# Kernel optimization log

Hardware: AMD Instinct MI355X
Metric: run time of the kernel (lower is better)

The kernel has to match this reference:

```python
import jax, jax.numpy as jnp
import numpy as np

NUM_HEADS = 16


def _local_attn(q, k, v, bias, nq, nk):
    """Blocked local attention, faithful to rearrange_to_dense_trunk semantics.
    q,k,v: [B,H,N,D]; bias: [B,Hb,N,N] (Hb broadcasts against H).
    Trunk i (queries [i*nq,(i+1)*nq)) attends keys at original indices
    [i*nq - pad_left, i*nq - pad_left + nk); out-of-range keys/values/bias are
    zero-padded (the module pads with zeros, no -inf key masking).
    Assumes N % nq == 0 (q_pad_length == 0, so the query mask loop is a no-op).
    """
    B, H, N, D = q.shape
    T = N // nq                      # n_trunks
    pad_left = (nk - nq) // 2
    Lp = (T - 1) * nq + nk           # padded key length so every window is full
    pad_right = Lp - pad_left - N
    k_p = jnp.pad(k, ((0, 0), (0, 0), (pad_left, pad_right), (0, 0)))
    v_p = jnp.pad(v, ((0, 0), (0, 0), (pad_left, pad_right), (0, 0)))
    b_p = jnp.pad(bias, ((0, 0), (0, 0), (0, 0), (pad_left, pad_right)))
    # window gather indices: [T, nk]
    kidx = jnp.arange(T)[:, None] * nq + jnp.arange(nk)[None, :]
    k_t = k_p[:, :, kidx, :]         # [B,H,T,nk,D]
    v_t = v_p[:, :, kidx, :]         # [B,H,T,nk,D]
    Bb, Hb = bias.shape[0], bias.shape[1]
    b_r = b_p.reshape(Bb, Hb, T, nq, Lp)
    b_t = jnp.take_along_axis(b_r, kidx[None, None, :, None, :], axis=-1)  # [Bb,Hb,T,nq,nk]
    q_t = q.reshape(B, H, T, nq, D)
    scores = jnp.einsum('bhtqd,bhtkd->bhtqk', q_t, k_t) + b_t
    w = jax.nn.softmax(scores, axis=-1)
    o = jnp.einsum('bhtqk,bhtkd->bhtqd', w, v_t)
    return o.reshape(B, H, N, D)


def setup_inputs() -> dict:
    key = jax.random.key(0)
    ks = jax.random.split(key, 8)
    B, N, C = 1, 4096, 256
    H, D = NUM_HEADS, 64
    HD = H * D
    q_x = jax.random.normal(ks[0], (B, N, C), dtype=jnp.float32)
    kv_x = jax.random.normal(ks[1], (B, N, C), dtype=jnp.float32)
    attn_bias = jax.random.normal(ks[2], (B, 1, N, N), dtype=jnp.float32) * 0.1
    Wq = jax.random.normal(ks[3], (C, HD), dtype=jnp.float32) / np.sqrt(C).astype(np.float32)
    Wk = jax.random.normal(ks[4], (C, HD), dtype=jnp.float32) / np.sqrt(C).astype(np.float32)
    Wv = jax.random.normal(ks[5], (C, HD), dtype=jnp.float32) / np.sqrt(C).astype(np.float32)
    Wg = jax.random.normal(ks[6], (C, HD), dtype=jnp.float32) / np.sqrt(C).astype(np.float32)
    Wo = jax.random.normal(ks[7], (HD, C), dtype=jnp.float32) / np.sqrt(HD).astype(np.float32)
    return {"q_x": q_x, "kv_x": kv_x, "attn_bias": attn_bias,
            "Wq": Wq, "Wk": Wk, "Wv": Wv, "Wg": Wg, "Wo": Wo,
            "n_queries": 64, "n_keys": 256}


def reference(q_x, kv_x, attn_bias, Wq, Wk, Wv, Wg, Wo, n_queries, n_keys):
    B, N, C = q_x.shape
    H = NUM_HEADS
    D = Wq.shape[-1] // H
    def split_heads(x):
        return x.reshape(B, N, H, D).transpose(0, 2, 1, 3)  # [B,H,N,D]
    q = split_heads(q_x @ Wq) / jnp.sqrt(jnp.float32(D))
    k = split_heads(kv_x @ Wk)
    v = split_heads(kv_x @ Wv)
    o = _local_attn(q, k, v, attn_bias, n_queries, n_keys)
    o = o.transpose(0, 2, 1, 3).reshape(B, N, H * D)
    g = jax.nn.sigmoid(q_x @ Wg)  # gating head
    return (o * g) @ Wo
```

## Files before the change

### kernel.cpp

```cpp
#include <hip/hip_runtime.h>

#define N_ 4096
#define C_ 256
#define H_ 16
#define D_ 64
#define HD_ 1024

typedef __attribute__((ext_vector_type(8))) _Float16 f16x8;
typedef __attribute__((ext_vector_type(4))) _Float16 f16x4;
typedef __attribute__((ext_vector_type(4))) float f32x4;

__device__ __forceinline__ void gload16(const void* g, void* l) {
    __builtin_amdgcn_global_load_lds(
        (const __attribute__((address_space(1))) unsigned int*)g,
        (__attribute__((address_space(3))) unsigned int*)l, 16, 0, 0);
}

__global__ __launch_bounds__(256) void convert_kernel(
    const float* __restrict__ q_x, const float* __restrict__ kv_x,
    const float* __restrict__ Wq, const float* __restrict__ Wk,
    const float* __restrict__ Wv, const float* __restrict__ Wg,
    const float* __restrict__ Wo,
    _Float16* __restrict__ Xf, _Float16* __restrict__ WTf,
    _Float16* __restrict__ WoTf)
{
    __shared__ float ts[64][65];
    const int b = blockIdx.x;
    const int tid = threadIdx.x;

    if (b < 512) {
        const int seg = b >> 8;
        const float* src = seg ? kv_x : q_x;
        _Float16* df = Xf + (size_t)seg * 1048576;
        const int base = (b & 255) * 4096 + tid * 16;
#pragma unroll
        for (int q = 0; q < 4; ++q) {
            float4 v = *(const float4*)&src[base + q * 4];
            f16x4 fv;
            fv[0] = (_Float16)v.x; fv[1] = (_Float16)v.y;
            fv[2] = (_Float16)v.z; fv[3] = (_Float16)v.w;
            *(f16x4*)&df[base + q * 4] = fv;
        }
        return;
    }

    const float* src;
    _Float16* df;
    int srcC, dstC, r0, c0;
    if (b < 768) {
        const int widx = (b - 512) >> 6;
        const int tile = (b - 512) & 63;
        src = (widx == 0) ? Wq : (widx == 1) ? Wk : (widx == 2) ? Wv : Wg;
        df = WTf + (size_t)widx * 262144;
        srcC = 1024; dstC = 256;
        r0 = (tile >> 4) * 64;
        c0 = (tile & 15) * 64;
    } else {
        const int tile = b - 768;
        src = Wo; df = WoTf;
        srcC = 256; dstC = 1024;
        r0 = (tile >> 2) * 64;
        c0 = (tile & 3) * 64;
    }
    {
        const int r = tid >> 2;
        const int cch = (tid & 3) * 16;
#pragma unroll
        for (int q = 0; q < 4; ++q) {
            float4 v = *(const float4*)&src[(size_t)(r0 + r) * srcC + c0 + cch + q * 4];
            ts[r][cch + q * 4 + 0] = v.x;
            ts[r][cch + q * 4 + 1] = v.y;
            ts[r][cch + q * 4 + 2] = v.z;
            ts[r][cch + q * 4 + 3] = v.w;
        }
    }
    __syncthreads();
    {
        const int c = tid >> 2;
        const int rch = (tid & 3) * 16;
#pragma unroll
        for (int q = 0; q < 4; ++q) {
            f16x4 fv;
#pragma unroll
            for (int j = 0; j < 4; ++j)
                fv[j] = (_Float16)ts[rch + q * 4 + j][c];
            *(f16x4*)&df[(size_t)(c0 + c) * dstC + r0 + rch + q * 4] = fv;
        }
    }
}

__global__ __launch_bounds__(256) void proj_mfma(
    const _Float16* __restrict__ Xf, const _Float16* __restrict__ WTf,
    _Float16* __restrict__ qh, _Float16* __restrict__ kh,
    _Float16* __restrict__ vh, _Float16* __restrict__ gh)
{
    __shared__ __align__(16) char psmem[34816];
    _Float16* As = (_Float16*)psmem;
    _Float16* Bs = (_Float16*)(psmem + 16384);

    const int lb  = blockIdx.x;
    const int xcd = lb & 7;
    const int gr  = (lb >> 6) * 8 + xcd;
    const int g   = gr >> 5;
    const int m0  = (gr & 31) * 128;
    const int c0  = ((lb >> 3) & 7) * 128;

    const _Float16* A = Xf + ((g == 1 || g == 2) ? 1048576 : 0);
    const _Float16* B = WTf + (size_t)g * 262144;

    const int tid  = threadIdx.x;
    const int wave = tid >> 6;
    const int lane = tid & 63;
    const int wr   = wave >> 1;
    const int wc   = wave & 1;
    const int frow = lane & 15;
    const int grp  = lane >> 4;

    f32x4 acc[4][4];
#pragma unroll
    for (int i = 0; i < 4; ++i)
#pragma unroll
        for (int j = 0; j < 4; ++j) acc[i][j] = (f32x4){0.f, 0.f, 0.f, 0.f};

    const int srow = tid >> 3;
    const int sch  = tid & 7;

    for (int kt = 0; kt < 256; kt += 64) {
        __syncthreads();
#pragma unroll
        for (int p = 0; p < 4; ++p) {
            const int row = p * 32 + srow;
            const int koff = kt + ((sch ^ (row & 7)) << 3);
            gload16(A + (size_t)(m0 + row) * 256 + koff, (char*)As + p * 4096 + tid * 16);
            gload16(B + (size_t)(c0 + row) * 256 + koff, (char*)Bs + p * 4096 + tid * 16);
        }
        __syncthreads();

#pragma unroll
        for (int ks = 0; ks < 2; ++ks) {
            f16x8 af[4], bf[4];
#pragma unroll
            for (int f = 0; f < 4; ++f) {
                const int ra = wr * 64 + f * 16 + frow;
                const int rb = wc * 64 + f * 16 + frow;
                af[f] = *(const f16x8*)((char*)As + ra * 128 + (((ks * 4 + grp) ^ (ra & 7)) << 4));
                bf[f] = *(const f16x8*)((char*)Bs + rb * 128 + (((ks * 4 + grp) ^ (rb & 7)) << 4));
            }
#pragma unroll
            for (int i = 0; i < 4; ++i)
#pragma unroll
                for (int j = 0; j < 4; ++j)
                    acc[i][j] = __builtin_amdgcn_mfma_f32_16x16x32_f16(af[i], bf[j], acc[i][j], 0, 0, 0);
        }
    }

    __syncthreads();
    _Float16* Epi = (_Float16*)psmem;
    {
        const float scale = (g == 0) ? 0.125f : 1.f;
#pragma unroll
        for (int i = 0; i < 4; ++i)
#pragma unroll
            for (int j = 0; j < 4; ++j) {
                const int rr = wr * 64 + i * 16 + grp * 4;
                const int cc = wc * 64 + j * 16 + frow;
#pragma unroll
                for (int v = 0; v < 4; ++v) {
                    float x = acc[i][j][v];
                    x = (g == 3) ? 1.f / (1.f + __expf(-x)) : x * scale;
                    Epi[(rr + v) * 136 + cc] = (_Float16)x;
                }
            }
    }
    __syncthreads();
    {
        const int ch   = tid & 15;
        const int head = ch >> 3;
        const int e8   = (ch & 7) * 8;
#pragma unroll
        for (int p = 0; p < 8; ++p) {
            const int r = p * 16 + (tid >> 4);
            const f16x8 val = *(const f16x8*)&Epi[r * 136 + head * 64 + e8];
            if (g == 3) {
                *(f16x8*)&gh[(size_t)(m0 + r) * HD_ + c0 + head * 64 + e8] = val;
            } else {
                _Float16* dst = (g == 0) ? qh : (g == 1) ? kh : vh;
                const int hh = (c0 >> 6) + head;
                *(f16x8*)&dst[((size_t)hh * N_ + m0 + r) * D_ + e8] = val;
            }
        }
    }
}

__global__ __launch_bounds__(256, 4) void attn_mfma(
    const _Float16* __restrict__ qh, const _Float16* __restrict__ kh,
    const _Float16* __restrict__ vh, const float* __restrict__ bias,
    const _Float16* __restrict__ gh, _Float16* __restrict__ of)
{
    __shared__ __align__(16) char smem[40960];
    _Float16* Qs = (_Float16*)smem;
    char* Ks = smem + 8192;
    _Float16* Ps = (_Float16*)smem;
    _Float16* Vs = (_Float16*)(smem + 17408);
    float* Oe = (float*)smem;

    const int lb  = blockIdx.x;
    const int xcd = lb & 7;
    const int j_  = lb >> 3;
    const int h   = j_ >> 3;
    const int t   = xcd * 8 + (j_ & 7);
    const int tid = threadIdx.x;
    const int lane = tid & 63;
    const int wv = tid >> 6;
    const int frow = lane & 15;
    const int grp = lane >> 4;
    const int kbase = t * 64 - 96;

    const char* qbase = (const char*)qh + (size_t)(h * N_ + t * 64) * 128;
    const char* kbase_p = (const char*)kh + (size_t)h * N_ * 128;

#pragma unroll
    for (int q = 0; q < 2; ++q) {
        const int lin = q * 4096 + tid * 16;
        const int row = lin >> 7;
        const int ch = (lin >> 4) & 7;
        gload16(qbase + row * 128 + ((ch ^ (row & 7)) << 4), (char*)Qs + lin);
    }
#pragma unroll
    for (int q = 0; q < 8; ++q) {
        const int lin = q * 4096 + tid * 16;
        const int row = lin >> 7;
        const int ch = (lin >> 4) & 7;
        const int kg = kbase + row;
        if ((unsigned)kg < (unsigned)N_) {
            gload16(kbase_p + (size_t)kg * 128 + ((ch ^ (row & 7)) << 4), Ks + lin);
        } else {
            *(float4*)(Ks + lin) = make_float4(0.f, 0.f, 0.f, 0.f);
        }
    }

    f32x4 sacc[16];
    {
        const int rowg = t * 64 + wv * 16 + grp * 4;
#pragma unroll
        for (int j = 0; j < 16; ++j) {
            const int colg = kbase + j * 16 + frow;
            const bool ok = (unsigned)colg < (unsigned)N_;
#pragma unroll
            for (int v = 0; v < 4; ++v)
                sacc[j][v] = ok ? bias[(size_t)(rowg + v) * N_ + colg] : 0.f;
        }
    }
    __syncthreads();

    {
        const int rq = wv * 16 + frow;
#pragma unroll
        for (int ks = 0; ks < 2; ++ks) {
            const f16x8 aq = *(const f16x8*)((char*)Qs + rq * 128 + (((ks * 4 + grp) ^ (rq & 7)) << 4));
#pragma unroll
            for (int j = 0; j < 16; ++j) {
                const int rk = j * 16 + frow;
                const f16x8 bk = *(const f16x8*)(Ks + rk * 128 + (((ks * 4 + grp) ^ (rk & 7)) << 4));
                sacc[j] = __builtin_amdgcn_mfma_f32_16x16x32_f16(aq, bk, sacc[j], 0, 0, 0);
            }
        }
    }
    __syncthreads();

    float inv[4];
#pragma unroll
    for (int v = 0; v < 4; ++v) {
        float m = sacc[0][v];
#pragma unroll
        for (int f = 1; f < 16; ++f) m = fmaxf(m, sacc[f][v]);
        m = fmaxf(m, __shfl_xor(m, 1));
        m = fmaxf(m, __shfl_xor(m, 2));
        m = fmaxf(m, __shfl_xor(m, 4));
        m = fmaxf(m, __shfl_xor(m, 8));
        float l = 0.f;
#pragma unroll
        for (int f = 0; f < 16; ++f) {
            float e = __expf(sacc[f][v] - m);
            sacc[f][v] = e;
            l += e;
        }
        l += __shfl_xor(l, 1);
        l += __shfl_xor(l, 2);
        l += __shfl_xor(l, 4);
        l += __shfl_xor(l, 8);
        inv[v] = 1.f / l;
    }

    f32x4 oacc[4];
#pragma unroll
    for (int jd = 0; jd < 4; ++jd) oacc[jd] = (f32x4){0.f, 0.f, 0.f, 0.f};

#pragma unroll
    for (int c = 0; c < 2; ++c) {
        {
            const int sl = tid >> 1;
            const int d0 = (tid & 1) * 32;
            const int kg = kbase + c * 128 + sl;
            f16x8 vv[4];
            if ((unsigned)kg < (unsigned)N_) {
                const f16x8* vp = (const f16x8*)(vh + ((size_t)h * N_ + kg) * D_ + d0);
#pragma unroll
                for (int q = 0; q < 4; ++q) vv[q] = vp[q];
            } else {
#pragma unroll
                for (int q = 0; q < 4; ++q)
#pragma unroll
                    for (int e = 0; e < 8; ++e) vv[q][e] = (_Float16)0.f;
            }
#pragma unroll
            for (int q = 0; q < 4; ++q)
#pragma unroll
                for (int e = 0; e < 8; ++e)
                    Vs[(d0 + q * 8 + e) * 136 + sl] = vv[q][e];
        }
        {
            const int rb = wv * 16 + grp * 4;
#pragma unroll
            for (int j = 0; j < 8; ++j) {
                const int col = j * 16 + frow;
#pragma unroll
                for (int v = 0; v < 4; ++v)
                    Ps[(rb + v) * 136 + col] = (_Float16)sacc[c * 8 + j][v];
            }
        }
        __syncthreads();
        const int rp = wv * 16 + frow;
#pragma unroll
        for (int ks = 0; ks < 4; ++ks) {
            const f16x8 ap = *(const f16x8*)((char*)Ps + rp * 272 + ks * 64 + grp * 16);
#pragma unroll
            for (int jd = 0; jd < 4; ++jd) {
                const f16x8 bv = *(const f16x8*)((char*)Vs + (jd * 16 + frow) * 272 + ks * 64 + grp * 16);
                oacc[jd] = __builtin_amdgcn_mfma_f32_16x16x32_f16(ap, bv, oacc[jd], 0, 0, 0);
            }
        }
        __syncthreads();
    }

#pragma unroll
    for (int jd = 0; jd < 4; ++jd) {
        const int dcol = jd * 16 + frow;
#pragma unroll
        for (int v = 0; v < 4; ++v) {
            const int rn = wv * 16 + grp * 4 + v;
            Oe[rn * 68 + dcol] = oacc[jd][v] * inv[v];
        }
    }
    __syncthreads();
    {
        const int r   = tid >> 2;
        const int seg = tid & 3;
        const int n   = t * 64 + r;
        const int cg0 = h * 64 + seg * 16;
        const float* orow = &Oe[r * 68 + seg * 16];
        f32x4 o0 = *(const f32x4*)&orow[0];
        f32x4 o1 = *(const f32x4*)&orow[4];
        f32x4 o2 = *(const f32x4*)&orow[8];
        f32x4 o3 = *(const f32x4*)&orow[12];
        const f16x8 g0 = *(const f16x8*)&gh[(size_t)n * HD_ + cg0];
        const f16x8 g1 = *(const f16x8*)&gh[(size_t)n * HD_ + cg0 + 8];
        f16x8 r0, r1;
#pragma unroll
        for (int e = 0; e < 4; ++e) {
            r0[e]     = (_Float16)(o0[e] * (float)g0[e]);
            r0[4 + e] = (_Float16)(o1[e] * (float)g0[4 + e]);
            r1[e]     = (_Float16)(o2[e] * (float)g1[e]);
            r1[4 + e] = (_Float16)(o3[e] * (float)g1[4 + e]);
        }
        *(f16x8*)&of[(size_t)n * HD_ + cg0]     = r0;
        *(f16x8*)&of[(size_t)n * HD_ + cg0 + 8] = r1;
    }
}

__global__ __launch_bounds__(256) void out_mfma(
    const _Float16* __restrict__ of, const _Float16* __restrict__ WoTf,
    float* __restrict__ out)
{
    __shared__ __align__(16) _Float16 smem[2048 + 4096];
    _Float16* As = smem;
    _Float16* Bs = smem + 2048;

    const int lb  = blockIdx.x;
    const int xcd = lb & 7;
    const int s   = lb >> 3;
    const int rowt = (s >> 2) * 8 + xcd;
    const int m0  = rowt * 32;
    const int c0  = (s & 3) * 64;

    const int tid  = threadIdx.x;
    const int wave = tid >> 6;
    const int lane = tid & 63;
    const int wr   = wave >> 1;
    const int wc   = wave & 1;
    const int frow = lane & 15;
    const int grp  = lane >> 4;

    f32x4 acc[2];
#pragma unroll
    for (int j = 0; j < 2; ++j) acc[j] = (f32x4){0.f, 0.f, 0.f, 0.f};

    for (int kt = 0; kt < 1024; kt += 64) {
        __syncthreads();
        {
            const int row = tid >> 3;
            const int ch  = tid & 7;
            const int koff = kt + ((ch ^ (row & 7)) << 3);
            gload16(of + (size_t)(m0 + row) * HD_ + koff, (char*)As + tid * 16);
        }
#pragma unroll
        for (int p = 0; p < 2; ++p) {
            const int lin = p * 4096 + tid * 16;
            const int row = lin >> 7;
            const int ch  = (lin >> 4) & 7;
            const int koff = kt + ((ch ^ (row & 7)) << 3);
            gload16(WoTf + (size_t)(c0 + row) * HD_ + koff, (char*)Bs + lin);
        }
        __syncthreads();

#pragma unroll
        for (int ks = 0; ks < 2; ++ks) {
            const int ra = wr * 16 + frow;
            const f16x8 af = *(const f16x8*)((char*)As + ra * 128 + (((ks * 4 + grp) ^ (ra & 7)) << 4));
#pragma unroll
            for (int j = 0; j < 2; ++j) {
                const int rb = wc * 32 + j * 16 + frow;
                const f16x8 bf = *(const f16x8*)((char*)Bs + rb * 128 + (((ks * 4 + grp) ^ (rb & 7)) << 4));
                acc[j] = __builtin_amdgcn_mfma_f32_16x16x32_f16(af, bf, acc[j], 0, 0, 0);
            }
        }
    }

    const int rbase = grp * 4;
#pragma unroll
    for (int j = 0; j < 2; ++j) {
        const int c = c0 + wc * 32 + j * 16 + frow;
#pragma unroll
        for (int v = 0; v < 4; ++v) {
            const int n = m0 + wr * 16 + rbase + v;
            out[(size_t)n * C_ + c] = acc[j][v];
        }
    }
}

extern "C" void kernel_launch(void* const* d_in, const int* in_sizes, int n_in,
                              void* d_out, int out_size, void* d_ws, size_t ws_size,
                              hipStream_t stream)
{
    const float* q_x  = (const float*)d_in[0];
    const float* kv_x = (const float*)d_in[1];
    const float* bias = (const float*)d_in[2];
    const float* Wq   = (const float*)d_in[3];
    const float* Wk   = (const float*)d_in[4];
    const float* Wv   = (const float*)d_in[5];
    const float* Wg   = (const float*)d_in[6];
    const float* Wo   = (const float*)d_in[7];
    float* out = (float*)d_out;

    char* ws = (char*)d_ws;
    const size_t MB = 1048576;
    _Float16* qh   = (_Float16*)(ws);
    _Float16* kh   = (_Float16*)(ws + 8  * MB);
    _Float16* vh   = (_Float16*)(ws + 16 * MB);
    _Float16* gh   = (_Float16*)(ws + 24 * MB);
    _Float16* of   = (_Float16*)(ws + 32 * MB);
    _Float16* Xf   = (_Float16*)(ws + 40 * MB);
    _Float16* WTf  = (_Float16*)(ws + 44 * MB);
    _Float16* WoTf = (_Float16*)(ws + 46 * MB);

    convert_kernel<<<832, 256, 0, stream>>>(q_x, kv_x, Wq, Wk, Wv, Wg, Wo,
                                            Xf, WTf, WoTf);
    proj_mfma<<<1024, 256, 0, stream>>>(Xf, WTf, qh, kh, vh, gh);
    attn_mfma<<<1024, 256, 0, stream>>>(qh, kh, vh, bias, gh, of);
    out_mfma<<<512, 256, 0, stream>>>(of, WoTf, out);
}
```

Baseline: 159.7 us.

## Fuse fp32-to-fp16 activation conversion into projection GEMM and vectorize V transpose

The separate pass that converted q_x and kv_x to fp16 is removed. The projection GEMM now reads fp32 activations directly, converts them in registers and writes fp16 into swizzled LDS, which saves a global write and re-read of the activations. In exchange, the A-tile loads become synchronous register loads instead of async global-to-LDS loads, and each block reloads the fp32 input for every column tile. Separately, the attention kernel's V transpose now has each thread load four key rows and write packed 4-wide fp16 vectors to LDS instead of scalar stores.

```diff
diff --git a/kernel.cpp b/kernel.cpp
--- a/kernel.cpp
+++ b/kernel.cpp
@@ -17,46 +17,28 @@
 }
 
 __global__ __launch_bounds__(256) void convert_kernel(
-    const float* __restrict__ q_x, const float* __restrict__ kv_x,
     const float* __restrict__ Wq, const float* __restrict__ Wk,
     const float* __restrict__ Wv, const float* __restrict__ Wg,
     const float* __restrict__ Wo,
-    _Float16* __restrict__ Xf, _Float16* __restrict__ WTf,
-    _Float16* __restrict__ WoTf)
+    _Float16* __restrict__ WTf, _Float16* __restrict__ WoTf)
 {
     __shared__ float ts[64][65];
     const int b = blockIdx.x;
     const int tid = threadIdx.x;
 
-    if (b < 512) {
-        const int seg = b >> 8;
-        const float* src = seg ? kv_x : q_x;
-        _Float16* df = Xf + (size_t)seg * 1048576;
-        const int base = (b & 255) * 4096 + tid * 16;
-#pragma unroll
-        for (int q = 0; q < 4; ++q) {
-            float4 v = *(const float4*)&src[base + q * 4];
-            f16x4 fv;
-            fv[0] = (_Float16)v.x; fv[1] = (_Float16)v.y;
-            fv[2] = (_Float16)v.z; fv[3] = (_Float16)v.w;
-            *(f16x4*)&df[base + q * 4] = fv;
-        }
-        return;
-    }
-
     const float* src;
     _Float16* df;
     int srcC, dstC, r0, c0;
-    if (b < 768) {
-        const int widx = (b - 512) >> 6;
-        const int tile = (b - 512) & 63;
+    if (b < 256) {
+        const int widx = b >> 6;
+        const int tile = b & 63;
         src = (widx == 0) ? Wq : (widx == 1) ? Wk : (widx == 2) ? Wv : Wg;
         df = WTf + (size_t)widx * 262144;
         srcC = 1024; dstC = 256;
         r0 = (tile >> 4) * 64;
         c0 = (tile & 15) * 64;
     } else {
-        const int tile = b - 768;
+        const int tile = b - 256;
         src = Wo; df = WoTf;
         srcC = 256; dstC = 1024;
         r0 = (tile >> 2) * 64;
@@ -90,7 +72,8 @@
 }
 
 __global__ __launch_bounds__(256) void proj_mfma(
-    const _Float16* __restrict__ Xf, const _Float16* __restrict__ WTf,
+    const float* __restrict__ q_x, const float* __restrict__ kv_x,
+    const _Float16* __restrict__ WTf,
     _Float16* __restrict__ qh, _Float16* __restrict__ kh,
     _Float16* __restrict__ vh, _Float16* __restrict__ gh)
 {
@@ -105,7 +88,7 @@
     const int m0  = (gr & 31) * 128;
     const int c0  = ((lb >> 3) & 7) * 128;
 
-    const _Float16* A = Xf + ((g == 1 || g == 2) ? 1048576 : 0);
+    const float* A32 = (g == 1 || g == 2) ? kv_x : q_x;
     const _Float16* B = WTf + (size_t)g * 262144;
 
     const int tid  = threadIdx.x;
@@ -131,8 +114,16 @@
         for (int p = 0; p < 4; ++p) {
             const int row = p * 32 + srow;
             const int koff = kt + ((sch ^ (row & 7)) << 3);
-            gload16(A + (size_t)(m0 + row) * 256 + koff, (char*)As + p * 4096 + tid * 16);
             gload16(B + (size_t)(c0 + row) * 256 + koff, (char*)Bs + p * 4096 + tid * 16);
+            const float* srcp = A32 + (size_t)(m0 + row) * 256 + koff;
+            float4 x0 = *(const float4*)srcp;
+            float4 x1 = *(const float4*)(srcp + 4);
+            f16x8 pk;
+            pk[0] = (_Float16)x0.x; pk[1] = (_Float16)x0.y;
+            pk[2] = (_Float16)x0.z; pk[3] = (_Float16)x0.w;
+            pk[4] = (_Float16)x1.x; pk[5] = (_Float16)x1.y;
+            pk[6] = (_Float16)x1.z; pk[7] = (_Float16)x1.w;
+            *(f16x8*)((char*)As + p * 4096 + tid * 16) = pk;
         }
         __syncthreads();
 
@@ -299,25 +290,28 @@
 #pragma unroll
     for (int c = 0; c < 2; ++c) {
         {
-            const int sl = tid >> 1;
-            const int d0 = (tid & 1) * 32;
-            const int kg = kbase + c * 128 + sl;
-            f16x8 vv[4];
-            if ((unsigned)kg < (unsigned)N_) {
-                const f16x8* vp = (const f16x8*)(vh + ((size_t)h * N_ + kg) * D_ + d0);
-#pragma unroll
-                for (int q = 0; q < 4; ++q) vv[q] = vp[q];
-            } else {
-#pragma unroll
-                for (int q = 0; q < 4; ++q)
-#pragma unroll
-                    for (int e = 0; e < 8; ++e) vv[q][e] = (_Float16)0.f;
-            }
-#pragma unroll
-            for (int q = 0; q < 4; ++q)
-#pragma unroll
-                for (int e = 0; e < 8; ++e)
-                    Vs[(d0 + q * 8 + e) * 136 + sl] = vv[q][e];
+            const int sg = tid >> 3;
+            const int dg = tid & 7;
+            const int s0 = sg * 4;
+            f16x8 vrow[4];
+#pragma unroll
+            for (int i = 0; i < 4; ++i) {
+                const int kg = kbase + c * 128 + s0 + i;
+                if ((unsigned)kg < (unsigned)N_) {
+                    vrow[i] = *(const f16x8*)(vh + ((size_t)h * N_ + kg) * D_ + dg * 8);
+                } else {
+#pragma unroll
+                    for (int e = 0; e < 8; ++e) vrow[i][e] = (_Float16)0.f;
+                }
+            }
+#pragma unroll
+            for (int e = 0; e < 8; ++e) {
+                const int d = dg * 8 + e;
+                f16x4 pk;
+                pk[0] = vrow[0][e]; pk[1] = vrow[1][e];
+                pk[2] = vrow[2][e]; pk[3] = vrow[3][e];
+                *(f16x4*)&Vs[d * 136 + s0] = pk;
+            }
         }
         {
             const int rb = wv * 16 + grp * 4;
@@ -469,13 +463,11 @@
     _Float16* vh   = (_Float16*)(ws + 16 * MB);
     _Float16* gh   = (_Float16*)(ws + 24 * MB);
     _Float16* of   = (_Float16*)(ws + 32 * MB);
-    _Float16* Xf   = (_Float16*)(ws + 40 * MB);
-    _Float16* WTf  = (_Float16*)(ws + 44 * MB);
-    _Float16* WoTf = (_Float16*)(ws + 46 * MB);
-
-    convert_kernel<<<832, 256, 0, stream>>>(q_x, kv_x, Wq, Wk, Wv, Wg, Wo,
-                                            Xf, WTf, WoTf);
-    proj_mfma<<<1024, 256, 0, stream>>>(Xf, WTf, qh, kh, vh, gh);
+    _Float16* WTf  = (_Float16*)(ws + 40 * MB);
+    _Float16* WoTf = (_Float16*)(ws + 42 * MB);
+
+    convert_kernel<<<320, 256, 0, stream>>>(Wq, Wk, Wv, Wg, Wo, WTf, WoTf);
+    proj_mfma<<<1024, 256, 0, stream>>>(q_x, kv_x, WTf, qh, kh, vh, gh);
     attn_mfma<<<1024, 256, 0, stream>>>(qh, kh, vh, bias, gh, of);
     out_mfma<<<512, 256, 0, stream>>>(of, WoTf, out);
 }
```

New measurement: 169.6 us. 6.2% more time.
